# Kernel tuning notes

Hardware: AMD Instinct MI355X
Metric: run time of the kernel (lower is better)

Reference implementation:

```python
import jax, jax.numpy as jnp
import numpy as np

EPS = 1e-6

def setup_inputs() -> dict:
    key = jax.random.key(0)
    ks = jax.random.split(key, 6)
    N, E, Din, H, D = 50000, 800000, 256, 4, 32
    x = jax.random.normal(ks[0], (N, Din), dtype=jnp.float32)
    adj_indices = jax.random.randint(ks[1], (E, 2), 0, N, dtype=jnp.int32)
    adj_weights = jax.random.uniform(ks[2], (E,), dtype=jnp.float32)
    W = jax.random.normal(ks[3], (Din, H * D), dtype=jnp.float32) * (1.0 / np.sqrt(Din))
    a_src = jax.random.normal(ks[4], (H, D), dtype=jnp.float32)
    a_dst = jax.random.normal(ks[5], (H, D), dtype=jnp.float32)
    return {"x": x, "adj_indices": adj_indices, "adj_weights": adj_weights,
            "W": W, "a_src": a_src, "a_dst": a_dst}

def reference(x, adj_indices, adj_weights, W, a_src, a_dst):
    N = x.shape[0]
    H, D = a_src.shape
    h = (x @ W).reshape(N, H, D)                       # [N,H,D]
    src = adj_indices[:, 0]
    dst = adj_indices[:, 1]
    hs = h[src]                                        # [E,H,D]
    hd = h[dst]                                        # [E,H,D]
    raw = jnp.einsum('ehd,hd->eh', hs, a_src) + jnp.einsum('ehd,hd->eh', hd, a_dst)
    gate = jnp.clip(adj_weights, EPS, None)[:, None]   # [E,1]
    scores = jnp.tanh(raw) + jnp.log(gate)             # [E,H]
    # per-destination segment softmax (numerically stable)
    seg_max = jax.ops.segment_max(scores, dst, num_segments=N)   # [N,H]
    ex = jnp.exp(scores - seg_max[dst])
    denom = jax.ops.segment_sum(ex, dst, num_segments=N)         # [N,H]
    alpha = ex / denom[dst]                            # softmax over edges per dst
    alpha = alpha * gate
    messages = alpha[:, :, None] * hs                  # [E,H,D]
    out = jax.ops.segment_sum(messages, dst, num_segments=N)     # [N,H,D]
    out = out.reshape(N, H * D)
    return jax.nn.gelu(out, approximate=False)
```

## Files before the change

### kernel.cpp

```cpp
#include <hip/hip_runtime.h>
#include <hip/hip_bf16.h>

#define N_NODES 50000
#define N_EDGES 800000
#define DIN 256
#define HD 128
#define NH 4
#define CAP 64
#define CSTR 16

#define GROWS 64
#define LDKH 136

#define GEMM_BLOCKS ((N_NODES + GROWS - 1) / GROWS)
#define SCAT_BLOCKS ((N_EDGES + 255) / 256)

typedef __bf16 bf16x8 __attribute__((ext_vector_type(8)));
typedef float  f32x4  __attribute__((ext_vector_type(4)));

static __device__ __forceinline__ unsigned short f2bu(float v) {
  union { __hip_bfloat16 b; unsigned short u; } c;
  c.b = __float2bfloat16(v);
  return c.u;
}

static __device__ __forceinline__ unsigned short f2hu(float v) {
  union { _Float16 h; unsigned short u; } c;
  c.h = (_Float16)v;
  return c.u;
}

static __device__ __forceinline__ float hu2f(unsigned short u) {
  union { _Float16 h; unsigned short u; } c;
  c.u = u;
  return (float)c.h;
}

__global__ void init_kernel(const float* __restrict__ W,
                            unsigned short* __restrict__ WtF,
                            int* __restrict__ cursor) {
  int i = blockIdx.x * 256 + threadIdx.x;
  if (i < HD * DIN) {
    int j    = i & 7;
    int lane = (i >> 3) & 63;
    int t    = (i >> 9) & 7;
    int s    = (i >> 12) & 3;
    int ks   = (i >> 14) & 1;
    int m = lane & 15, q = lane >> 4;
    int k = ks * 128 + 32 * s + 8 * q + j;
    int c = 16 * t + m;
    WtF[i] = f2bu(W[k * HD + c]);
  }
  if (i < N_NODES * CSTR) cursor[i] = 0;
}

__global__ void fused_gemm_scatter(
    const float* __restrict__ x,
    const unsigned short* __restrict__ WtF,
    const float* __restrict__ a_src,
    const float* __restrict__ a_dst,
    unsigned short* __restrict__ hbf,
    float* __restrict__ ssrc,
    float* __restrict__ sdst,
    const int2* __restrict__ adj,
    const float* __restrict__ wts,
    int* __restrict__ cursor,
    unsigned int* __restrict__ slots) {
  __shared__ unsigned short xs[GROWS * LDKH];
  const int tid = threadIdx.x;

  if (blockIdx.x >= GEMM_BLOCKS) {
    int e = (blockIdx.x - GEMM_BLOCKS) * 256 + tid;
    if (e >= N_EDGES) return;
    int2 sd = adj[e];
    if ((unsigned)sd.x >= (unsigned)N_NODES || (unsigned)sd.y >= (unsigned)N_NODES) return;
    float g = fmaxf(wts[e], 1e-6f);
    int pos = atomicAdd(&cursor[sd.y * CSTR], 1);
    if (pos >= CAP) pos = CAP - 1;
    unsigned packed = ((unsigned)f2hu(g) << 16) | (unsigned)(sd.x & 0xffff);
    __builtin_nontemporal_store(packed, &slots[((size_t)sd.y << 6) + pos]);
    return;
  }

  const int row0 = blockIdx.x * GROWS;
  const int wid  = tid >> 6;
  const int lane = tid & 63;
  const int m    = lane & 15;
  const int q    = lane >> 4;

  float4 v0[8];
#pragma unroll
  for (int it = 0; it < 8; it++) {
    int i = it * 256 + tid, r = i >> 5, kq = i & 31;
    int row = row0 + r;
    v0[it] = (row < N_NODES) ? *(const float4*)(x + (size_t)row * DIN + 4 * kq)
                             : make_float4(0.f, 0.f, 0.f, 0.f);
  }
#pragma unroll
  for (int it = 0; it < 8; it++) {
    int i = it * 256 + tid, r = i >> 5, kq = i & 31;
    ushort4 b;
    b.x = f2bu(v0[it].x); b.y = f2bu(v0[it].y); b.z = f2bu(v0[it].z); b.w = f2bu(v0[it].w);
    *(ushort4*)&xs[r * LDKH + 4 * kq] = b;
  }
  __syncthreads();

  f32x4 acc[8];
#pragma unroll
  for (int t = 0; t < 8; t++) acc[t] = (f32x4){0.f, 0.f, 0.f, 0.f};

  const unsigned short* xbase = &xs[(wid * 16 + m) * LDKH];

  bf16x8 a0[4];
#pragma unroll
  for (int s = 0; s < 4; s++) a0[s] = *(const bf16x8*)(xbase + 32 * s + 8 * q);

  float4 v1[8];
#pragma unroll
  for (int it = 0; it < 8; it++) {
    int i = it * 256 + tid, r = i >> 5, kq = i & 31;
    int row = row0 + r;
    v1[it] = (row < N_NODES) ? *(const float4*)(x + (size_t)row * DIN + 128 + 4 * kq)
                             : make_float4(0.f, 0.f, 0.f, 0.f);
  }

#pragma unroll
  for (int s = 0; s < 4; s++) {
    bf16x8 bfr[8];
#pragma unroll
    for (int t = 0; t < 8; t++)
      bfr[t] = *(const bf16x8*)(WtF + (size_t)((0 * 4 + s) * 8 + t) * 512 + lane * 8);
#pragma unroll
    for (int t = 0; t < 8; t++)
      acc[t] = __builtin_amdgcn_mfma_f32_16x16x32_bf16(a0[s], bfr[t], acc[t], 0, 0, 0);
  }
  __syncthreads();

#pragma unroll
  for (int it = 0; it < 8; it++) {
    int i = it * 256 + tid, r = i >> 5, kq = i & 31;
    ushort4 b;
    b.x = f2bu(v1[it].x); b.y = f2bu(v1[it].y); b.z = f2bu(v1[it].z); b.w = f2bu(v1[it].w);
    *(ushort4*)&xs[r * LDKH + 4 * kq] = b;
  }
  __syncthreads();

  bf16x8 a1[4];
#pragma unroll
  for (int s = 0; s < 4; s++) a1[s] = *(const bf16x8*)(xbase + 32 * s + 8 * q);

#pragma unroll
  for (int s = 0; s < 4; s++) {
    bf16x8 bfr[8];
#pragma unroll
    for (int t = 0; t < 8; t++)
      bfr[t] = *(const bf16x8*)(WtF + (size_t)((1 * 4 + s) * 8 + t) * 512 + lane * 8);
#pragma unroll
    for (int t = 0; t < 8; t++)
      acc[t] = __builtin_amdgcn_mfma_f32_16x16x32_bf16(a1[s], bfr[t], acc[t], 0, 0, 0);
  }

#pragma unroll
  for (int t = 0; t < 8; t++) {
#pragma unroll
    for (int r = 0; r < 4; r++) {
      int row = row0 + wid * 16 + q * 4 + r;
      if (row < N_NODES) hbf[(size_t)row * HD + 16 * t + m] = f2bu(acc[t][r]);
    }
  }

  float as[8], ad[8];
#pragma unroll
  for (int t = 0; t < 8; t++) {
    as[t] = a_src[16 * t + m];
    ad[t] = a_dst[16 * t + m];
  }
#pragma unroll
  for (int r = 0; r < 4; r++) {
    float ps[NH] = {0.f, 0.f, 0.f, 0.f};
    float pd[NH] = {0.f, 0.f, 0.f, 0.f};
#pragma unroll
    for (int t = 0; t < 8; t++) {
      ps[t >> 1] = fmaf(acc[t][r], as[t], ps[t >> 1]);
      pd[t >> 1] = fmaf(acc[t][r], ad[t], pd[t >> 1]);
    }
#pragma unroll
    for (int mm = 8; mm >= 1; mm >>= 1) {
#pragma unroll
      for (int hh = 0; hh < NH; hh++) {
        ps[hh] += __shfl_xor(ps[hh], mm, 64);
        pd[hh] += __shfl_xor(pd[hh], mm, 64);
      }
    }
    int row = row0 + wid * 16 + q * 4 + r;
    if (m == 0 && row < N_NODES) {
#pragma unroll
      for (int hh = 0; hh < NH; hh++) {
        ssrc[row * NH + hh] = ps[hh];
        sdst[row * NH + hh] = pd[hh];
      }
    }
  }
}

__global__ __launch_bounds__(128, 4) void node_kernel(
    const int* __restrict__ cursor,
    const unsigned int* __restrict__ slots,
    const float4* __restrict__ ssrc4,
    const float4* __restrict__ sdst4,
    const unsigned int* __restrict__ hbf32,
    float* __restrict__ out) {
  const int tid  = threadIdx.x;
  const int wid  = tid >> 6;
  const int lane = tid & 63;
  const int n    = blockIdx.x * 2 + wid;
  const int hh   = lane >> 4;

  int deg = cursor[n * CSTR];
  if (deg > CAP) deg = CAP;

  __shared__ int    sidx[2][CAP];
  __shared__ float4 swv[2][CAP];

  float4 ex = make_float4(0.f, 0.f, 0.f, 0.f);
  if (lane < deg) {
    unsigned sl = slots[((size_t)n << 6) + lane];
    int s = (int)(sl & 0xffffu);
    float g = hu2f((unsigned short)(sl >> 16));
    float4 ss = ssrc4[s];
    float4 sd = sdst4[n];
    ex.x = g * expf(tanhf(ss.x + sd.x));
    ex.y = g * expf(tanhf(ss.y + sd.y));
    ex.z = g * expf(tanhf(ss.z + sd.z));
    ex.w = g * expf(tanhf(ss.w + sd.w));
    sidx[wid][lane] = s;
    swv[wid][lane] = make_float4(ex.x * g, ex.y * g, ex.z * g, ex.w * g);
  }

  float4 tot = ex;
#pragma unroll
  for (int mm = 32; mm >= 1; mm >>= 1) {
    tot.x += __shfl_xor(tot.x, mm, 64);
    tot.y += __shfl_xor(tot.y, mm, 64);
    tot.z += __shfl_xor(tot.z, mm, 64);
    tot.w += __shfl_xor(tot.w, mm, 64);
  }
  float dn  = (hh == 0) ? tot.x : (hh == 1) ? tot.y : (hh == 2) ? tot.z : tot.w;
  float inv = (dn > 0.f) ? 1.f / dn : 0.f;
  __syncthreads();

  float acc0 = 0.f, acc1 = 0.f;
  int j = 0;
  for (; j + 8 <= deg; j += 8) {
    int s0 = sidx[wid][j + 0], s1 = sidx[wid][j + 1];
    int s2 = sidx[wid][j + 2], s3 = sidx[wid][j + 3];
    int s4 = sidx[wid][j + 4], s5 = sidx[wid][j + 5];
    int s6 = sidx[wid][j + 6], s7 = sidx[wid][j + 7];
    unsigned u0 = hbf32[(size_t)s0 * (HD / 2) + lane];
    unsigned u1 = hbf32[(size_t)s1 * (HD / 2) + lane];
    unsigned u2 = hbf32[(size_t)s2 * (HD / 2) + lane];
    unsigned u3 = hbf32[(size_t)s3 * (HD / 2) + lane];
    unsigned u4 = hbf32[(size_t)s4 * (HD / 2) + lane];
    unsigned u5 = hbf32[(size_t)s5 * (HD / 2) + lane];
    unsigned u6 = hbf32[(size_t)s6 * (HD / 2) + lane];
    unsigned u7 = hbf32[(size_t)s7 * (HD / 2) + lane];
    float w0 = ((const float*)&swv[wid][j + 0])[hh];
    float w1 = ((const float*)&swv[wid][j + 1])[hh];
    float w2 = ((const float*)&swv[wid][j + 2])[hh];
    float w3 = ((const float*)&swv[wid][j + 3])[hh];
    float w4 = ((const float*)&swv[wid][j + 4])[hh];
    float w5 = ((const float*)&swv[wid][j + 5])[hh];
    float w6 = ((const float*)&swv[wid][j + 6])[hh];
    float w7 = ((const float*)&swv[wid][j + 7])[hh];
    acc0 = fmaf(w0, __uint_as_float(u0 << 16), acc0);
    acc1 = fmaf(w0, __uint_as_float(u0 & 0xffff0000u), acc1);
    acc0 = fmaf(w1, __uint_as_float(u1 << 16), acc0);
    acc1 = fmaf(w1, __uint_as_float(u1 & 0xffff0000u), acc1);
    acc0 = fmaf(w2, __uint_as_float(u2 << 16), acc0);
    acc1 = fmaf(w2, __uint_as_float(u2 & 0xffff0000u), acc1);
    acc0 = fmaf(w3, __uint_as_float(u3 << 16), acc0);
    acc1 = fmaf(w3, __uint_as_float(u3 & 0xffff0000u), acc1);
    acc0 = fmaf(w4, __uint_as_float(u4 << 16), acc0);
    acc1 = fmaf(w4, __uint_as_float(u4 & 0xffff0000u), acc1);
    acc0 = fmaf(w5, __uint_as_float(u5 << 16), acc0);
    acc1 = fmaf(w5, __uint_as_float(u5 & 0xffff0000u), acc1);
    acc0 = fmaf(w6, __uint_as_float(u6 << 16), acc0);
    acc1 = fmaf(w6, __uint_as_float(u6 & 0xffff0000u), acc1);
    acc0 = fmaf(w7, __uint_as_float(u7 << 16), acc0);
    acc1 = fmaf(w7, __uint_as_float(u7 & 0xffff0000u), acc1);
  }
  for (; j < deg; j++) {
    int s0 = sidx[wid][j];
    unsigned u0 = hbf32[(size_t)s0 * (HD / 2) + lane];
    float w0 = ((const float*)&swv[wid][j])[hh];
    acc0 = fmaf(w0, __uint_as_float(u0 << 16), acc0);
    acc1 = fmaf(w0, __uint_as_float(u0 & 0xffff0000u), acc1);
  }
  acc0 *= inv;
  acc1 *= inv;

  float2 gl;
  gl.x = 0.5f * acc0 * (1.f + erff(acc0 * 0.70710678118654752f));
  gl.y = 0.5f * acc1 * (1.f + erff(acc1 * 0.70710678118654752f));
  *(float2*)&out[(size_t)n * HD + 2 * lane] = gl;
}

extern "C" void kernel_launch(void* const* d_in, const int* in_sizes, int n_in,
                              void* d_out, int out_size, void* d_ws, size_t ws_size,
                              hipStream_t stream) {
  const float* x     = (const float*)d_in[0];
  const int2*  adj   = (const int2*)d_in[1];
  const float* wts   = (const float*)d_in[2];
  const float* W     = (const float*)d_in[3];
  const float* a_src = (const float*)d_in[4];
  const float* a_dst = (const float*)d_in[5];
  float* out = (float*)d_out;

  char* p = (char*)d_ws;
  auto carve = [&](size_t bytes) {
    char* q = p;
    p += (bytes + 255) & ~(size_t)255;
    return (void*)q;
  };
  unsigned short* hbf = (unsigned short*)carve((size_t)N_NODES * HD * sizeof(unsigned short));
  unsigned short* WtF = (unsigned short*)carve((size_t)HD * DIN * sizeof(unsigned short));
  float* ssrc   = (float*)carve((size_t)N_NODES * NH * sizeof(float));
  float* sdst   = (float*)carve((size_t)N_NODES * NH * sizeof(float));
  unsigned int* slots = (unsigned int*)carve((size_t)N_NODES * CAP * sizeof(unsigned int));
  int*   cursor = (int*)carve((size_t)N_NODES * CSTR * sizeof(int));

  init_kernel<<<(N_NODES * CSTR + 255) / 256, 256, 0, stream>>>(W, WtF, cursor);
  fused_gemm_scatter<<<GEMM_BLOCKS + SCAT_BLOCKS, 256, 0, stream>>>(
      x, WtF, a_src, a_dst, hbf, ssrc, sdst, adj, wts, cursor, slots);
  node_kernel<<<N_NODES / 2, 128, 0, stream>>>(cursor, slots, (const float4*)ssrc,
                                               (const float4*)sdst,
                                               (const unsigned int*)hbf, out);
}
```

Before: 192.3 us.

## Prefetch first eight neighbor rows early, memset cursor, add launch bounds

New measurement: 197.0 us. +2.5%, slower.

```diff
diff --git a/kernel.cpp b/kernel.cpp
--- a/kernel.cpp
+++ b/kernel.cpp
@@ -37,8 +37,7 @@
 }
 
 __global__ void init_kernel(const float* __restrict__ W,
-                            unsigned short* __restrict__ WtF,
-                            int* __restrict__ cursor) {
+                            unsigned short* __restrict__ WtF) {
   int i = blockIdx.x * 256 + threadIdx.x;
   if (i < HD * DIN) {
     int j    = i & 7;
@@ -51,10 +50,9 @@
     int c = 16 * t + m;
     WtF[i] = f2bu(W[k * HD + c]);
   }
-  if (i < N_NODES * CSTR) cursor[i] = 0;
-}
-
-__global__ void fused_gemm_scatter(
+}
+
+__global__ __launch_bounds__(256, 2) void fused_gemm_scatter(
     const float* __restrict__ x,
     const unsigned short* __restrict__ WtF,
     const float* __restrict__ a_src,
@@ -222,18 +220,40 @@
   __shared__ int    sidx[2][CAP];
   __shared__ float4 swv[2][CAP];
 
+  unsigned sl = 0;
+  if (lane < deg) sl = slots[((size_t)n << 6) + lane];
+  int myS = (int)(sl & 0xffffu);
+
+  unsigned pu0 = 0, pu1 = 0, pu2 = 0, pu3 = 0, pu4 = 0, pu5 = 0, pu6 = 0, pu7 = 0;
+  {
+    int b0 = __shfl(myS, 0, 64) & 0xffff;
+    int b1 = __shfl(myS, 1, 64) & 0xffff;
+    int b2 = __shfl(myS, 2, 64) & 0xffff;
+    int b3 = __shfl(myS, 3, 64) & 0xffff;
+    int b4 = __shfl(myS, 4, 64) & 0xffff;
+    int b5 = __shfl(myS, 5, 64) & 0xffff;
+    int b6 = __shfl(myS, 6, 64) & 0xffff;
+    int b7 = __shfl(myS, 7, 64) & 0xffff;
+    pu0 = hbf32[(size_t)b0 * (HD / 2) + lane];
+    pu1 = hbf32[(size_t)b1 * (HD / 2) + lane];
+    pu2 = hbf32[(size_t)b2 * (HD / 2) + lane];
+    pu3 = hbf32[(size_t)b3 * (HD / 2) + lane];
+    pu4 = hbf32[(size_t)b4 * (HD / 2) + lane];
+    pu5 = hbf32[(size_t)b5 * (HD / 2) + lane];
+    pu6 = hbf32[(size_t)b6 * (HD / 2) + lane];
+    pu7 = hbf32[(size_t)b7 * (HD / 2) + lane];
+  }
+
   float4 ex = make_float4(0.f, 0.f, 0.f, 0.f);
   if (lane < deg) {
-    unsigned sl = slots[((size_t)n << 6) + lane];
-    int s = (int)(sl & 0xffffu);
     float g = hu2f((unsigned short)(sl >> 16));
-    float4 ss = ssrc4[s];
+    float4 ss = ssrc4[myS];
     float4 sd = sdst4[n];
     ex.x = g * expf(tanhf(ss.x + sd.x));
     ex.y = g * expf(tanhf(ss.y + sd.y));
     ex.z = g * expf(tanhf(ss.z + sd.z));
     ex.w = g * expf(tanhf(ss.w + sd.w));
-    sidx[wid][lane] = s;
+    sidx[wid][lane] = myS;
     swv[wid][lane] = make_float4(ex.x * g, ex.y * g, ex.z * g, ex.w * g);
   }
 
@@ -250,7 +270,21 @@
   __syncthreads();
 
   float acc0 = 0.f, acc1 = 0.f;
-  int j = 0;
+
+  {
+    int dlim = (deg < 8) ? deg : 8;
+    unsigned pus[8] = {pu0, pu1, pu2, pu3, pu4, pu5, pu6, pu7};
+#pragma unroll
+    for (int j = 0; j < 8; j++) {
+      if (j < dlim) {
+        float wj = ((const float*)&swv[wid][j])[hh];
+        acc0 = fmaf(wj, __uint_as_float(pus[j] << 16), acc0);
+        acc1 = fmaf(wj, __uint_as_float(pus[j] & 0xffff0000u), acc1);
+      }
+    }
+  }
+
+  int j = 8;
   for (; j + 8 <= deg; j += 8) {
     int s0 = sidx[wid][j + 0], s1 = sidx[wid][j + 1];
     int s2 = sidx[wid][j + 2], s3 = sidx[wid][j + 3];
@@ -329,7 +363,8 @@
   unsigned int* slots = (unsigned int*)carve((size_t)N_NODES * CAP * sizeof(unsigned int));
   int*   cursor = (int*)carve((size_t)N_NODES * CSTR * sizeof(int));
 
-  init_kernel<<<(N_NODES * CSTR + 255) / 256, 256, 0, stream>>>(W, WtF, cursor);
+  hipMemsetAsync(cursor, 0, (size_t)N_NODES * CSTR * sizeof(int), stream);
+  init_kernel<<<(HD * DIN + 255) / 256, 256, 0, stream>>>(W, WtF);
   fused_gemm_scatter<<<GEMM_BLOCKS + SCAT_BLOCKS, 256, 0, stream>>>(
       x, WtF, a_src, a_dst, hbf, ssrc, sdst, adj, wts, cursor, slots);
   node_kernel<<<N_NODES / 2, 128, 0, stream>>>(cursor, slots, (const float4*)ssrc,
```
